# Kernel optimization log

Hardware: AMD Instinct MI355X
Metric: run time of the kernel (lower is better)

Reference implementation:

```python
import jax, jax.numpy as jnp
import numpy as np

B, H, S, D = 2, 16, 2048, 128


def _fp8_roundtrip(x):
    # Simulate fp8 e4m3fnuz storage: values are exactly representable in fp8.
    return x.astype(jnp.float8_e4m3fnuz).astype(jnp.float32)


def setup_inputs() -> dict:
    key = jax.random.key(0)
    k0, k1, k2, k3, k4, k5, k6 = jax.random.split(key, 7)
    q = _fp8_roundtrip(jax.random.normal(k0, (B, H, S, D), jnp.float32))
    k = _fp8_roundtrip(jax.random.normal(k1, (B, H, S, D), jnp.float32))
    v = _fp8_roundtrip(jax.random.normal(k2, (B, H, S, D), jnp.float32))
    # per-tensor dequant scales (positive)
    qs = jax.random.uniform(k3, (1,), jnp.float32, 0.5, 1.5)
    ks = jax.random.uniform(k4, (1,), jnp.float32, 0.5, 1.5)
    vs = jax.random.uniform(k5, (1,), jnp.float32, 0.5, 1.5)
    s = jax.random.normal(k6, (1,), jnp.float32)  # unused by forward (kept for signature fidelity)
    return {"s": s, "q": q, "k": k, "v": v, "qs": qs, "ks": ks, "vs": vs}


def reference(s, q, k, v, qs, ks, vs):
    # Dequantize fp8 tensors with per-tensor scales, then standard SDPA.
    qd = q * qs  # (B,H,S,D)
    kd = k * ks
    vd = v * vs
    scale = 1.0 / np.sqrt(D).astype(np.float32)
    logits = jnp.einsum('bhqd,bhkd->bhqk', qd, kd) * scale  # (B,H,S,S)
    attn = jax.nn.softmax(logits, axis=-1)
    return jnp.einsum('bhqk,bhkd->bhqd', attn, vd)  # (B,H,S,D)
```

## Files before the change

kernel.cpp:

```cpp
#include <hip/hip_runtime.h>


#define S_LEN 2048
#define D_DIM 128
#define BM 128
#define BN 64
#define NT (S_LEN / BN)
#define LDQB 136
#define LDKB 136
#define LDP 72
#define LDV 72
#define VROWS 144

typedef _Float16 half8   __attribute__((ext_vector_type(8)));
typedef _Float16 half4_t __attribute__((ext_vector_type(4)));
typedef float    floatx4 __attribute__((ext_vector_type(4)));

__device__ __forceinline__ long pk8_fp8(const float4 a, const float4 b) {
    unsigned int w0 = __builtin_amdgcn_cvt_pk_fp8_f32(a.x, a.y, 0u, false);
    w0 = (unsigned int)__builtin_amdgcn_cvt_pk_fp8_f32(a.z, a.w, w0, true);
    unsigned int w1 = __builtin_amdgcn_cvt_pk_fp8_f32(b.x, b.y, 0u, false);
    w1 = (unsigned int)__builtin_amdgcn_cvt_pk_fp8_f32(b.z, b.w, w1, true);
    return (long)(((unsigned long long)w1 << 32) | (unsigned long long)w0);
}

__global__ __launch_bounds__(512, 4)
void fa_fwd(const float* __restrict__ qg, const float* __restrict__ kg,
            const float* __restrict__ vg, const float* __restrict__ qsp,
            const float* __restrict__ ksp, const float* __restrict__ vsp,
            float* __restrict__ outg)
{
    __shared__ __align__(16) unsigned char QsPhRaw[BM * LDP * 2];
    __shared__ __align__(16) unsigned char Ksf2[2][BN * LDKB];
    __shared__ __align__(16) _Float16 Vt2[2][VROWS * LDV];

    const int tid  = threadIdx.x;
    const int wave = tid >> 6;
    const int lane = tid & 63;
    const int l16  = lane & 15;
    const int quad = lane >> 4;

    const int bid = blockIdx.x;
    const int bh  = ((bid & 7) << 2) + (bid >> 7);
    const int qb  = (bid >> 3) & 15;
    const int q0  = qb * BM;
    const size_t base = (size_t)bh * (S_LEN * D_DIM);

    const float sks    = qsp[0] * ksp[0];
    const float scale  = sks * 0.08838834764831845f;
    const float negM   = -4.0f * sks;
    const float vscale = vsp[0];

    const int c8  = (tid & 15) << 3;
    const int r0  = tid >> 4;
    const int tq  = tid & 15;
    const int cg0 = (tid >> 4) << 2;

    const float* kbase = kg + base;
    const float* vbase = vg + base;

    float4 kr[4], vr[4];
    auto load_tile = [&](int kt) {
        const float* kb = kbase + (size_t)(kt * BN) * D_DIM;
        const float* vb = vbase + (size_t)(kt * BN) * D_DIM;
        #pragma unroll
        for (int i = 0; i < 2; ++i) {
            const float* src = kb + (size_t)(r0 + 32 * i) * D_DIM + c8;
            kr[2 * i]     = *(const float4*)src;
            kr[2 * i + 1] = *(const float4*)(src + 4);
        }
        #pragma unroll
        for (int u = 0; u < 4; ++u)
            vr[u] = *(const float4*)(vb + (size_t)(tq + 16 * u) * D_DIM + cg0);
    };
    auto store_tile = [&](int b) {
        #pragma unroll
        for (int i = 0; i < 2; ++i)
            *(long*)&Ksf2[b][(r0 + 32 * i) * LDKB + c8] = pk8_fp8(kr[2 * i], kr[2 * i + 1]);
        #pragma unroll
        for (int j = 0; j < 4; ++j) {
            const int d = cg0 + j;
            half4_t h = { (_Float16)((const float*)&vr[0])[j],
                          (_Float16)((const float*)&vr[1])[j],
                          (_Float16)((const float*)&vr[2])[j],
                          (_Float16)((const float*)&vr[3])[j] };
            *(half4_t*)&Vt2[b][d * LDV + 4 * tq] = h;
        }
    };

    load_tile(0);

    {
        unsigned char* QsF = QsPhRaw;
        for (int r = r0; r < BM; r += 32) {
            const float* src = qg + base + (size_t)(q0 + r) * D_DIM + c8;
            const float4 f0 = *(const float4*)src;
            const float4 f1 = *(const float4*)(src + 4);
            *(long*)&QsF[r * LDQB + c8] = pk8_fp8(f0, f1);
        }
        for (int i = tid; i < (VROWS - D_DIM) * LDV; i += 512) {
            const _Float16 v = (i < LDV) ? (_Float16)1.0f : (_Float16)0.0f;
            Vt2[0][D_DIM * LDV + i] = v;
            Vt2[1][D_DIM * LDV + i] = v;
        }
    }
    __syncthreads();

    long qf[4];
    {
        const unsigned char* QsF = QsPhRaw;
        #pragma unroll
        for (int d0 = 0; d0 < 4; ++d0)
            qf[d0] = *(const long*)&QsF[(wave * 16 + l16) * LDQB + d0 * 32 + quad * 8];
    }
    _Float16* const Ph = (_Float16*)QsPhRaw;

    store_tile(0);
    load_tile(1);

    floatx4 o_acc[9];
    #pragma unroll
    for (int c = 0; c < 9; ++c) o_acc[c] = (floatx4){0.f, 0.f, 0.f, 0.f};

    for (int kt = 0; kt < NT; ++kt) {
        __syncthreads();
        if (kt + 1 < NT) store_tile((kt + 1) & 1);
        if (kt + 2 < NT) load_tile(kt + 2);

        const unsigned char* const Kst = Ksf2[kt & 1];
        const _Float16*      const Vtt = Vt2[kt & 1];

        floatx4 sacc[4];
        #pragma unroll
        for (int n = 0; n < 4; ++n) sacc[n] = (floatx4){0.f, 0.f, 0.f, 0.f};
        #pragma unroll
        for (int n = 0; n < 4; ++n) {
            #pragma unroll
            for (int d0 = 0; d0 < 4; ++d0) {
                const long kf = *(const long*)&Kst[(n * 16 + l16) * LDKB + d0 * 32 + quad * 8];
                sacc[n] = __builtin_amdgcn_mfma_f32_16x16x32_fp8_fp8(qf[d0], kf, sacc[n], 0, 0, 0);
            }
        }

        #pragma unroll
        for (int rg = 0; rg < 4; ++rg) {
            half4_t ph4;
            #pragma unroll
            for (int n = 0; n < 4; ++n)
                ph4[n] = (_Float16)__expf(fmaf(sacc[n][rg], scale, negM));
            const int row = wave * 16 + quad * 4 + rg;
            *(half4_t*)&Ph[row * LDP + 4 * l16] = ph4;
        }

        #pragma unroll
        for (int k0 = 0; k0 < 2; ++k0) {
            const half8 af = *(const half8*)&Ph[(wave * 16 + l16) * LDP + k0 * 32 + quad * 8];
            #pragma unroll
            for (int c = 0; c < 9; ++c) {
                const int d = c * 16 + l16;
                const half8 bf = *(const half8*)&Vtt[d * LDV + k0 * 32 + quad * 8];
                o_acc[c] = __builtin_amdgcn_mfma_f32_16x16x32_f16(af, bf, o_acc[c], 0, 0, 0);
            }
        }
    }

    #pragma unroll
    for (int rg = 0; rg < 4; ++rg) {
        const float l    = __shfl(o_acc[8][rg], lane & 48);
        const float invl = vscale / l;
        const int row = q0 + wave * 16 + quad * 4 + rg;
        float* orow = outg + base + (size_t)row * D_DIM;
        #pragma unroll
        for (int c = 0; c < 8; ++c)
            orow[c * 16 + l16] = o_acc[c][rg] * invl;
    }
}

extern "C" void kernel_launch(void* const* d_in, const int* in_sizes, int n_in,
                              void* d_out, int out_size, void* d_ws, size_t ws_size,
                              hipStream_t stream) {
    const float* q  = (const float*)d_in[1];
    const float* k  = (const float*)d_in[2];
    const float* v  = (const float*)d_in[3];
    const float* qs = (const float*)d_in[4];
    const float* ks = (const float*)d_in[5];
    const float* vs = (const float*)d_in[6];
    float* out = (float*)d_out;

    fa_fwd<<<dim3(512), 512, 0, stream>>>(q, k, v, qs, ks, vs, out);
}
```

Measured before the change: 215.8 us.

## Split waves into 32-row groups sharing key and output-column halves

Each wave now owns 32 query rows (two M-fragments) and half of the key columns for QK^T, and half of the output columns for PV. Each K and V fragment read from LDS then feeds two MFMAs instead of one, which cuts shared-memory read traffic per MFMA. Waves now depend on each other's P tiles, so an extra __syncthreads is added each iteration. The row-sum column is computed redundantly by both waves of a pair, adding a couple of MFMAs.

```diff
diff --git a/kernel.cpp b/kernel.cpp
--- a/kernel.cpp
+++ b/kernel.cpp
@@ -14,6 +14,7 @@
 
 typedef _Float16 half8   __attribute__((ext_vector_type(8)));
 typedef _Float16 half4_t __attribute__((ext_vector_type(4)));
+typedef _Float16 half2_t __attribute__((ext_vector_type(2)));
 typedef float    floatx4 __attribute__((ext_vector_type(4)));
 
 __device__ __forceinline__ long pk8_fp8(const float4 a, const float4 b) {
@@ -39,6 +40,8 @@
     const int lane = tid & 63;
     const int l16  = lane & 15;
     const int quad = lane >> 4;
+    const int rowg = wave >> 1;
+    const int kh   = wave & 1;
 
     const int bid = blockIdx.x;
     const int bh  = ((bid & 7) << 2) + (bid >> 7);
@@ -106,21 +109,25 @@
     }
     __syncthreads();
 
-    long qf[4];
+    long qf[2][4];
     {
         const unsigned char* QsF = QsPhRaw;
         #pragma unroll
-        for (int d0 = 0; d0 < 4; ++d0)
-            qf[d0] = *(const long*)&QsF[(wave * 16 + l16) * LDQB + d0 * 32 + quad * 8];
+        for (int mf = 0; mf < 2; ++mf)
+            #pragma unroll
+            for (int d0 = 0; d0 < 4; ++d0)
+                qf[mf][d0] = *(const long*)&QsF[(rowg * 32 + mf * 16 + l16) * LDQB + d0 * 32 + quad * 8];
     }
     _Float16* const Ph = (_Float16*)QsPhRaw;
 
     store_tile(0);
     load_tile(1);
 
-    floatx4 o_acc[9];
+    floatx4 o_acc[2][5];
     #pragma unroll
-    for (int c = 0; c < 9; ++c) o_acc[c] = (floatx4){0.f, 0.f, 0.f, 0.f};
+    for (int mf = 0; mf < 2; ++mf)
+        #pragma unroll
+        for (int ci = 0; ci < 5; ++ci) o_acc[mf][ci] = (floatx4){0.f, 0.f, 0.f, 0.f};
 
     for (int kt = 0; kt < NT; ++kt) {
         __syncthreads();
@@ -130,49 +137,65 @@
         const unsigned char* const Kst = Ksf2[kt & 1];
         const _Float16*      const Vtt = Vt2[kt & 1];
 
-        floatx4 sacc[4];
-        #pragma unroll
-        for (int n = 0; n < 4; ++n) sacc[n] = (floatx4){0.f, 0.f, 0.f, 0.f};
-        #pragma unroll
-        for (int n = 0; n < 4; ++n) {
+        floatx4 sacc[2][2];
+        #pragma unroll
+        for (int mf = 0; mf < 2; ++mf)
+            #pragma unroll
+            for (int nn = 0; nn < 2; ++nn) sacc[mf][nn] = (floatx4){0.f, 0.f, 0.f, 0.f};
+        #pragma unroll
+        for (int nn = 0; nn < 2; ++nn) {
             #pragma unroll
             for (int d0 = 0; d0 < 4; ++d0) {
-                const long kf = *(const long*)&Kst[(n * 16 + l16) * LDKB + d0 * 32 + quad * 8];
-                sacc[n] = __builtin_amdgcn_mfma_f32_16x16x32_fp8_fp8(qf[d0], kf, sacc[n], 0, 0, 0);
-            }
-        }
-
-        #pragma unroll
-        for (int rg = 0; rg < 4; ++rg) {
-            half4_t ph4;
-            #pragma unroll
-            for (int n = 0; n < 4; ++n)
-                ph4[n] = (_Float16)__expf(fmaf(sacc[n][rg], scale, negM));
-            const int row = wave * 16 + quad * 4 + rg;
-            *(half4_t*)&Ph[row * LDP + 4 * l16] = ph4;
-        }
+                const long kf = *(const long*)&Kst[((2 * kh + nn) * 16 + l16) * LDKB + d0 * 32 + quad * 8];
+                sacc[0][nn] = __builtin_amdgcn_mfma_f32_16x16x32_fp8_fp8(qf[0][d0], kf, sacc[0][nn], 0, 0, 0);
+                sacc[1][nn] = __builtin_amdgcn_mfma_f32_16x16x32_fp8_fp8(qf[1][d0], kf, sacc[1][nn], 0, 0, 0);
+            }
+        }
+
+        #pragma unroll
+        for (int mf = 0; mf < 2; ++mf) {
+            #pragma unroll
+            for (int rg = 0; rg < 4; ++rg) {
+                half2_t p2;
+                p2[0] = (_Float16)__expf(fmaf(sacc[mf][0][rg], scale, negM));
+                p2[1] = (_Float16)__expf(fmaf(sacc[mf][1][rg], scale, negM));
+                const int row = rowg * 32 + mf * 16 + quad * 4 + rg;
+                *(half2_t*)&Ph[row * LDP + 4 * l16 + 2 * kh] = p2;
+            }
+        }
+        __syncthreads();
 
         #pragma unroll
         for (int k0 = 0; k0 < 2; ++k0) {
-            const half8 af = *(const half8*)&Ph[(wave * 16 + l16) * LDP + k0 * 32 + quad * 8];
-            #pragma unroll
-            for (int c = 0; c < 9; ++c) {
+            half8 af[2];
+            #pragma unroll
+            for (int mf = 0; mf < 2; ++mf)
+                af[mf] = *(const half8*)&Ph[(rowg * 32 + mf * 16 + l16) * LDP + k0 * 32 + quad * 8];
+            #pragma unroll
+            for (int ci = 0; ci < 5; ++ci) {
+                const int c = (ci < 4) ? (kh * 4 + ci) : 8;
                 const int d = c * 16 + l16;
                 const half8 bf = *(const half8*)&Vtt[d * LDV + k0 * 32 + quad * 8];
-                o_acc[c] = __builtin_amdgcn_mfma_f32_16x16x32_f16(af, bf, o_acc[c], 0, 0, 0);
+                o_acc[0][ci] = __builtin_amdgcn_mfma_f32_16x16x32_f16(af[0], bf, o_acc[0][ci], 0, 0, 0);
+                o_acc[1][ci] = __builtin_amdgcn_mfma_f32_16x16x32_f16(af[1], bf, o_acc[1][ci], 0, 0, 0);
             }
         }
     }
 
     #pragma unroll
-    for (int rg = 0; rg < 4; ++rg) {
-        const float l    = __shfl(o_acc[8][rg], lane & 48);
-        const float invl = vscale / l;
-        const int row = q0 + wave * 16 + quad * 4 + rg;
-        float* orow = outg + base + (size_t)row * D_DIM;
-        #pragma unroll
-        for (int c = 0; c < 8; ++c)
-            orow[c * 16 + l16] = o_acc[c][rg] * invl;
+    for (int mf = 0; mf < 2; ++mf) {
+        #pragma unroll
+        for (int rg = 0; rg < 4; ++rg) {
+            const float l    = __shfl(o_acc[mf][4][rg], lane & 48);
+            const float invl = vscale / l;
+            const int row = q0 + rowg * 32 + mf * 16 + quad * 4 + rg;
+            float* orow = outg + base + (size_t)row * D_DIM;
+            #pragma unroll
+            for (int ci = 0; ci < 4; ++ci) {
+                const int c = kh * 4 + ci;
+                orow[c * 16 + l16] = o_acc[mf][ci][rg] * invl;
+            }
+        }
     }
 }
 
```

New measurement: 218.1 us. Within noise of the previous version (+1.1%).

## Keep P in registers via transposed QK^T, drop P LDS staging, software-pipeline PV

Applied to the files above, without the earlier changes.

QK^T now runs with K as the A operand, so each lane's accumulators already have the A-fragment layout of the PV MFMA. P can therefore be packed straight into registers with no round-trip through shared memory, and V is stored with a matching permuted k-order. The row sum is computed explicitly with cross-lane shuffles instead of the ones-column trick, which removes the ninth accumulator and 16 rows of V. V becomes triple-buffered so the PV step for tile kt-1 overlaps the QK^T of tile kt; the freed P buffer space now holds Q staging. exp switches to exp2 with pre-folded log2e.

```diff
diff --git a/kernel.cpp b/kernel.cpp
--- a/kernel.cpp
+++ b/kernel.cpp
@@ -8,12 +8,12 @@
 #define NT (S_LEN / BN)
 #define LDQB 136
 #define LDKB 136
-#define LDP 72
 #define LDV 72
-#define VROWS 144
+#define VROWS 128
 
 typedef _Float16 half8   __attribute__((ext_vector_type(8)));
 typedef _Float16 half4_t __attribute__((ext_vector_type(4)));
+typedef _Float16 half2_t __attribute__((ext_vector_type(2)));
 typedef float    floatx4 __attribute__((ext_vector_type(4)));
 
 __device__ __forceinline__ long pk8_fp8(const float4 a, const float4 b) {
@@ -30,9 +30,8 @@
             const float* __restrict__ ksp, const float* __restrict__ vsp,
             float* __restrict__ outg)
 {
-    __shared__ __align__(16) unsigned char QsPhRaw[BM * LDP * 2];
     __shared__ __align__(16) unsigned char Ksf2[2][BN * LDKB];
-    __shared__ __align__(16) _Float16 Vt2[2][VROWS * LDV];
+    __shared__ __align__(16) _Float16 Vt3[3][VROWS * LDV];
 
     const int tid  = threadIdx.x;
     const int wave = tid >> 6;
@@ -47,36 +46,40 @@
     const size_t base = (size_t)bh * (S_LEN * D_DIM);
 
     const float sks    = qsp[0] * ksp[0];
-    const float scale  = sks * 0.08838834764831845f;
-    const float negM   = -4.0f * sks;
+    const float scale2 = sks * 0.08838834764831845f * 1.44269504088896f;
+    const float negM2  = -4.0f * sks * 1.44269504088896f;
     const float vscale = vsp[0];
 
     const int c8  = (tid & 15) << 3;
     const int r0  = tid >> 4;
-    const int tq  = tid & 15;
-    const int cg0 = (tid >> 4) << 2;
+    const int g    = tid & 15;
+    const int nn_s = g >> 2;
+    const int t2   = g & 3;
+    const int r4   = nn_s * 16 + t2 * 4;
+    const int kb   = (nn_s >> 1) * 32 + t2 * 8 + (nn_s & 1) * 4;
+    const int cg0  = (tid >> 4) << 2;
 
     const float* kbase = kg + base;
     const float* vbase = vg + base;
 
     float4 kr[4], vr[4];
     auto load_tile = [&](int kt) {
-        const float* kb = kbase + (size_t)(kt * BN) * D_DIM;
-        const float* vb = vbase + (size_t)(kt * BN) * D_DIM;
+        const float* kbp = kbase + (size_t)(kt * BN) * D_DIM;
+        const float* vbp = vbase + (size_t)(kt * BN) * D_DIM;
         #pragma unroll
         for (int i = 0; i < 2; ++i) {
-            const float* src = kb + (size_t)(r0 + 32 * i) * D_DIM + c8;
+            const float* src = kbp + (size_t)(r0 + 32 * i) * D_DIM + c8;
             kr[2 * i]     = *(const float4*)src;
             kr[2 * i + 1] = *(const float4*)(src + 4);
         }
         #pragma unroll
         for (int u = 0; u < 4; ++u)
-            vr[u] = *(const float4*)(vb + (size_t)(tq + 16 * u) * D_DIM + cg0);
+            vr[u] = *(const float4*)(vbp + (size_t)(r4 + u) * D_DIM + cg0);
     };
-    auto store_tile = [&](int b) {
+    auto store_tile = [&](int kbuf, int vbuf) {
         #pragma unroll
         for (int i = 0; i < 2; ++i)
-            *(long*)&Ksf2[b][(r0 + 32 * i) * LDKB + c8] = pk8_fp8(kr[2 * i], kr[2 * i + 1]);
+            *(long*)&Ksf2[kbuf][(r0 + 32 * i) * LDKB + c8] = pk8_fp8(kr[2 * i], kr[2 * i + 1]);
         #pragma unroll
         for (int j = 0; j < 4; ++j) {
             const int d = cg0 + j;
@@ -84,95 +87,114 @@
                           (_Float16)((const float*)&vr[1])[j],
                           (_Float16)((const float*)&vr[2])[j],
                           (_Float16)((const float*)&vr[3])[j] };
-            *(half4_t*)&Vt2[b][d * LDV + 4 * tq] = h;
+            *(half4_t*)&Vt3[vbuf][d * LDV + kb] = h;
         }
     };
 
     load_tile(0);
 
     {
-        unsigned char* QsF = QsPhRaw;
+        unsigned char* QsF = (unsigned char*)&Vt3[2][0];
         for (int r = r0; r < BM; r += 32) {
             const float* src = qg + base + (size_t)(q0 + r) * D_DIM + c8;
             const float4 f0 = *(const float4*)src;
             const float4 f1 = *(const float4*)(src + 4);
             *(long*)&QsF[r * LDQB + c8] = pk8_fp8(f0, f1);
         }
-        for (int i = tid; i < (VROWS - D_DIM) * LDV; i += 512) {
-            const _Float16 v = (i < LDV) ? (_Float16)1.0f : (_Float16)0.0f;
-            Vt2[0][D_DIM * LDV + i] = v;
-            Vt2[1][D_DIM * LDV + i] = v;
-        }
     }
     __syncthreads();
 
     long qf[4];
     {
-        const unsigned char* QsF = QsPhRaw;
+        const unsigned char* QsF = (const unsigned char*)&Vt3[2][0];
         #pragma unroll
         for (int d0 = 0; d0 < 4; ++d0)
             qf[d0] = *(const long*)&QsF[(wave * 16 + l16) * LDQB + d0 * 32 + quad * 8];
     }
-    _Float16* const Ph = (_Float16*)QsPhRaw;
-
-    store_tile(0);
+
+    store_tile(0, 0);
     load_tile(1);
 
-    floatx4 o_acc[9];
+    floatx4 o_acc[8];
     #pragma unroll
-    for (int c = 0; c < 9; ++c) o_acc[c] = (floatx4){0.f, 0.f, 0.f, 0.f};
+    for (int c = 0; c < 8; ++c) o_acc[c] = (floatx4){0.f, 0.f, 0.f, 0.f};
+    float l_acc = 0.0f;
+
+    half8 af0, af1;
+    int vb_st = 1;
+    int vb_pv = 2;
+
+    auto pv_step = [&](const _Float16* Vtt) {
+        #pragma unroll
+        for (int k0 = 0; k0 < 2; ++k0) {
+            const half8 af = k0 ? af1 : af0;
+            #pragma unroll
+            for (int ci = 0; ci < 8; ++ci) {
+                const half8 bf = *(const half8*)&Vtt[(ci * 16 + l16) * LDV + k0 * 32 + quad * 8];
+                o_acc[ci] = __builtin_amdgcn_mfma_f32_16x16x32_f16(af, bf, o_acc[ci], 0, 0, 0);
+            }
+        }
+    };
 
     for (int kt = 0; kt < NT; ++kt) {
         __syncthreads();
-        if (kt + 1 < NT) store_tile((kt + 1) & 1);
+        if (kt + 1 < NT) store_tile((kt + 1) & 1, vb_st);
         if (kt + 2 < NT) load_tile(kt + 2);
 
         const unsigned char* const Kst = Ksf2[kt & 1];
-        const _Float16*      const Vtt = Vt2[kt & 1];
 
         floatx4 sacc[4];
         #pragma unroll
-        for (int n = 0; n < 4; ++n) sacc[n] = (floatx4){0.f, 0.f, 0.f, 0.f};
-        #pragma unroll
-        for (int n = 0; n < 4; ++n) {
+        for (int nn = 0; nn < 4; ++nn) sacc[nn] = (floatx4){0.f, 0.f, 0.f, 0.f};
+        #pragma unroll
+        for (int nn = 0; nn < 4; ++nn) {
             #pragma unroll
             for (int d0 = 0; d0 < 4; ++d0) {
-                const long kf = *(const long*)&Kst[(n * 16 + l16) * LDKB + d0 * 32 + quad * 8];
-                sacc[n] = __builtin_amdgcn_mfma_f32_16x16x32_fp8_fp8(qf[d0], kf, sacc[n], 0, 0, 0);
+                const long kf = *(const long*)&Kst[(nn * 16 + l16) * LDKB + d0 * 32 + quad * 8];
+                sacc[nn] = __builtin_amdgcn_mfma_f32_16x16x32_fp8_fp8(kf, qf[d0], sacc[nn], 0, 0, 0);
             }
         }
 
-        #pragma unroll
-        for (int rg = 0; rg < 4; ++rg) {
-            half4_t ph4;
+        if (kt > 0) pv_step(&Vt3[vb_pv][0]);
+
+        {
+            union { half8 h8; half2_t h2[4]; } ua, ub;
+            float lsum = 0.0f;
             #pragma unroll
-            for (int n = 0; n < 4; ++n)
-                ph4[n] = (_Float16)__expf(fmaf(sacc[n][rg], scale, negM));
-            const int row = wave * 16 + quad * 4 + rg;
-            *(half4_t*)&Ph[row * LDP + 4 * l16] = ph4;
-        }
-
-        #pragma unroll
-        for (int k0 = 0; k0 < 2; ++k0) {
-            const half8 af = *(const half8*)&Ph[(wave * 16 + l16) * LDP + k0 * 32 + quad * 8];
-            #pragma unroll
-            for (int c = 0; c < 9; ++c) {
-                const int d = c * 16 + l16;
-                const half8 bf = *(const half8*)&Vtt[d * LDV + k0 * 32 + quad * 8];
-                o_acc[c] = __builtin_amdgcn_mfma_f32_16x16x32_f16(af, bf, o_acc[c], 0, 0, 0);
+            for (int nn = 0; nn < 4; ++nn) {
+                #pragma unroll
+                for (int pr = 0; pr < 2; ++pr) {
+                    const float e0 = exp2f(fmaf(sacc[nn][2 * pr],     scale2, negM2));
+                    const float e1 = exp2f(fmaf(sacc[nn][2 * pr + 1], scale2, negM2));
+                    half2_t h = { (_Float16)e0, (_Float16)e1 };
+                    lsum += (float)h[0] + (float)h[1];
+                    if (nn < 2) ua.h2[(nn & 1) * 2 + pr] = h;
+                    else        ub.h2[(nn & 1) * 2 + pr] = h;
+                }
             }
-        }
-    }
+            af0 = ua.h8;
+            af1 = ub.h8;
+            lsum += __shfl_xor(lsum, 16);
+            lsum += __shfl_xor(lsum, 32);
+            l_acc += lsum;
+        }
+
+        vb_st = (vb_st == 2) ? 0 : vb_st + 1;
+        vb_pv = (vb_pv == 2) ? 0 : vb_pv + 1;
+    }
+
+    pv_step(&Vt3[vb_pv][0]);
 
     #pragma unroll
     for (int rg = 0; rg < 4; ++rg) {
-        const float l    = __shfl(o_acc[8][rg], lane & 48);
-        const float invl = vscale / l;
-        const int row = q0 + wave * 16 + quad * 4 + rg;
+        const int r = quad * 4 + rg;
+        const float lv   = __shfl(l_acc, (lane & 48) | r);
+        const float invl = vscale / lv;
+        const int row = q0 + wave * 16 + r;
         float* orow = outg + base + (size_t)row * D_DIM;
         #pragma unroll
-        for (int c = 0; c < 8; ++c)
-            orow[c * 16 + l16] = o_acc[c][rg] * invl;
+        for (int ci = 0; ci < 8; ++ci)
+            orow[ci * 16 + l16] = o_acc[ci][rg] * invl;
     }
 }
 
```

Measured after the change: 240.8 us. +11.6%, slower.
